# Optimization experiments

Measured on AMD Instinct MI355X. Metric: run time of the kernel, lower is better.

Reference implementation:

```python
import jax, jax.numpy as jnp
import numpy as np

B, L, H, E, F, C = 8, 8192, 512, 8, 1024, 2  # batch, seq, hidden, experts, ffn, capacity factor


def setup_inputs() -> dict:
    key = jax.random.key(0)
    ks = jax.random.split(key, 4)
    x = jax.random.normal(ks[0], (B, L, H), jnp.float32)
    Wg = jax.random.normal(ks[1], (H, E), jnp.float32) * (H ** -0.5)   # gate (no bias)
    W1 = jax.random.normal(ks[2], (E, H, F), jnp.float32) * (H ** -0.5)
    b1 = jnp.zeros((E, F), jnp.float32)
    W2 = jax.random.normal(ks[3], (E, F, H), jnp.float32) * (F ** -0.5)
    b2 = jnp.zeros((E, H), jnp.float32)
    return {"x": x, "Wg": Wg, "W1": W1, "b1": b1, "W2": W2, "b2": b2}


def reference(x, Wg, W1, b1, W2, b2):
    b, l, h = x.shape
    e = Wg.shape[1]
    k = min(max(int(l * C / e), 1), l)  # expert-choice capacity per expert
    # Gate scores: softmax over experts per token, then each expert picks its top-k tokens.
    S = jax.nn.softmax(x @ Wg, axis=-1)          # (b, l, E)
    St = jnp.swapaxes(S, 1, 2)                   # (b, E, l)
    G, I = jax.lax.top_k(St, k)                  # (b, E, k) scores / token indices
    # Dispatch: gather each expert's chosen tokens.
    ex = jnp.take_along_axis(x[:, None], I[..., None], axis=2)   # (b, E, k, h)
    # Grouped expert MLP (Linear -> GELU -> Linear), batched over experts.
    hmid = jax.nn.gelu(jnp.einsum('bekh,ehf->bekf', ex, W1) + b1[None, :, None, :],
                       approximate=False)
    out = jnp.einsum('bekf,efh->bekh', hmid, W2) + b2[None, :, None, :]
    vals = G[..., None] * out                    # weight by gate score
    # Combine: scatter-add expert outputs back to token positions.
    new_x = jnp.zeros_like(x).at[jnp.arange(b)[:, None, None], I].add(vals)
    return new_x
```

## Files before the change

### kernel.cpp

```cpp
#include <hip/hip_runtime.h>
#include <hip/hip_bf16.h>
#include <hip/hip_fp16.h>

typedef float f32x4 __attribute__((ext_vector_type(4)));
typedef _Float16 f16x8 __attribute__((ext_vector_type(8)));
typedef unsigned int u32x4 __attribute__((ext_vector_type(4)));

static constexpr int Bb = 8, Ll = 8192, Hh = 512, Ee = 8, Ff = 1024, KK = 2048;

static __device__ __forceinline__ float fast_rcp(float x) {
#if __has_builtin(__builtin_amdgcn_rcpf)
  return __builtin_amdgcn_rcpf(x);
#else
  return 1.0f / x;
#endif
}

static __device__ __forceinline__ float gelu_exact(float v) {
  float a = __builtin_fabsf(v) * 0.70710678118654752f;
  float t = fast_rcp(__builtin_fmaf(0.3275911f, a, 1.0f));
  float p = __builtin_fmaf(1.061405429f, t, -1.453152027f);
  p = __builtin_fmaf(p, t, 1.421413741f);
  p = __builtin_fmaf(p, t, -0.284496736f);
  p = __builtin_fmaf(p, t, 0.254829592f);
  p = p * t;
  float e = __expf(-a * a);
  float er = __builtin_fmaf(-p, e, 1.0f);
  er = __builtin_copysignf(er, v);
  return 0.5f * v * (1.0f + er);
}

static __device__ __forceinline__ void nt_store16(const f16x8& v, _Float16* p) {
  __builtin_nontemporal_store(*reinterpret_cast<const u32x4*>(&v),
                              reinterpret_cast<u32x4*>(p));
}

__global__ __launch_bounds__(256) void transpose_cvt_kernel(const float* __restrict__ src,
                                                            _Float16* __restrict__ dst,
                                                            int R, int C) {
  __shared__ float tile[32][33];
  int z = blockIdx.z;
  const float* s = src + (size_t)z * R * C;
  _Float16* d = dst + (size_t)z * R * C;
  int c0 = blockIdx.x * 32, r0 = blockIdx.y * 32;
  int tx = threadIdx.x, ty = threadIdx.y;
#pragma unroll
  for (int i = ty; i < 32; i += 8) tile[i][tx] = s[(size_t)(r0 + i) * C + (c0 + tx)];
  __syncthreads();
#pragma unroll
  for (int i = ty; i < 32; i += 8) d[(size_t)(c0 + i) * R + (r0 + tx)] = (_Float16)tile[tx][i];
}

__global__ __launch_bounds__(256) void gatecvt_kernel(const float* __restrict__ x,
                                                      const float* __restrict__ Wg,
                                                      double* __restrict__ St,
                                                      _Float16* __restrict__ xb) {
  __shared__ float wgt[8][516];
  __shared__ float xs[32][68];
  int tid = threadIdx.x;
  for (int i = tid; i < Hh * Ee; i += 256) wgt[i & 7][i >> 3] = Wg[i];
  int row = tid >> 3, seg = tid & 7;
  int tl = row, e = seg;
  int token0 = blockIdx.x * 32;
  const float* xrow = x + (size_t)(token0 + row) * Hh;
  _Float16* xbrow = xb + (size_t)(token0 + row) * Hh;
  float4 r0 = reinterpret_cast<const float4*>(xrow)[seg * 2];
  float4 r1 = reinterpret_cast<const float4*>(xrow)[seg * 2 + 1];
  double acc = 0.0;
  for (int c = 0; c < 8; ++c) {
    f16x8 h;
    h[0] = (_Float16)r0.x; h[1] = (_Float16)r0.y; h[2] = (_Float16)r0.z; h[3] = (_Float16)r0.w;
    h[4] = (_Float16)r1.x; h[5] = (_Float16)r1.y; h[6] = (_Float16)r1.z; h[7] = (_Float16)r1.w;
    nt_store16(h, xbrow + c * 64 + seg * 8);
    __syncthreads();
    *reinterpret_cast<float4*>(&xs[row][seg * 8]) = r0;
    *reinterpret_cast<float4*>(&xs[row][seg * 8 + 4]) = r1;
    if (c + 1 < 8) {
      r0 = reinterpret_cast<const float4*>(xrow + (c + 1) * 64)[seg * 2];
      r1 = reinterpret_cast<const float4*>(xrow + (c + 1) * 64)[seg * 2 + 1];
    }
    __syncthreads();
#pragma unroll
    for (int hh = 0; hh < 64; hh += 4) {
      float4 xv = *reinterpret_cast<const float4*>(&xs[tl][hh]);
      float4 wv = *reinterpret_cast<const float4*>(&wgt[e][c * 64 + hh]);
      acc += (double)xv.x * (double)wv.x;
      acc += (double)xv.y * (double)wv.y;
      acc += (double)xv.z * (double)wv.z;
      acc += (double)xv.w * (double)wv.w;
    }
  }
  double m = acc;
  m = fmax(m, __shfl_xor(m, 1, 64));
  m = fmax(m, __shfl_xor(m, 2, 64));
  m = fmax(m, __shfl_xor(m, 4, 64));
  double ex = exp(acc - m);
  double s = ex;
  s += __shfl_xor(s, 1, 64);
  s += __shfl_xor(s, 2, 64);
  s += __shfl_xor(s, 4, 64);
  int token = token0 + tl;
  int b = token >> 13, l = token & (Ll - 1);
  St[((size_t)(b * Ee + e)) * Ll + l] = ex / s;
}

__global__ __launch_bounds__(1024) void topk_kernel(const double* __restrict__ St,
                                                    int* __restrict__ idx,
                                                    float* __restrict__ gate) {
  __shared__ unsigned long long keys[Ll];
  __shared__ unsigned int hist[256];
  __shared__ unsigned int sc[1024];
  __shared__ unsigned long long s_prefix;
  __shared__ int s_remaining;
  __shared__ unsigned long long redA[16], redO[16];
  int row = blockIdx.x;
  int tid = threadIdx.x;
  const double* s = St + (size_t)row * Ll;
  unsigned long long myA = ~0ULL, myO = 0ULL;
  for (int i = tid; i < Ll; i += 1024) {
    unsigned long long kx = (unsigned long long)__double_as_longlong(s[i]);
    keys[i] = kx;
    myA &= kx;
    myO |= kx;
  }
#pragma unroll
  for (int off2 = 32; off2 >= 1; off2 >>= 1) {
    myA &= __shfl_xor(myA, off2, 64);
    myO |= __shfl_xor(myO, off2, 64);
  }
  if ((tid & 63) == 0) { redA[tid >> 6] = myA; redO[tid >> 6] = myO; }
  __syncthreads();
  unsigned long long allA = redA[0], allO = redO[0];
#pragma unroll
  for (int w = 1; w < 16; ++w) { allA &= redA[w]; allO |= redO[w]; }
  unsigned long long diff = allA ^ allO;

  unsigned long long T;
  int nEqTake;
  if (diff == 0) {
    T = allA;
    nEqTake = KK;
  } else {
    int hb = 63 - __builtin_clzll(diff);
    int pv = hb >> 3;
    unsigned long long prefmask = (pv >= 7) ? 0ULL : (~0ULL << ((pv + 1) * 8));
    unsigned long long prefix = allA & prefmask;
    int remaining = KK;
    for (int p = pv; p >= 0; --p) {
      if (tid < 256) hist[tid] = 0;
      __syncthreads();
      int sh = p * 8;
      for (int i = tid; i < Ll; i += 1024) {
        unsigned long long kk = keys[i];
        if ((kk & prefmask) == prefix) atomicAdd(&hist[(unsigned)(kk >> sh) & 255u], 1u);
      }
      __syncthreads();
      if (tid < 256) sc[tid] = hist[tid];
      __syncthreads();
#pragma unroll
      for (int off = 1; off < 256; off <<= 1) {
        unsigned v = (tid < 256 && tid + off < 256) ? sc[tid + off] : 0;
        __syncthreads();
        if (tid < 256) sc[tid] += v;
        __syncthreads();
      }
      if (tid < 256) {
        unsigned incl = sc[tid];
        unsigned above = (tid == 255) ? 0u : sc[tid + 1];
        if ((int)incl >= remaining && (int)above < remaining) {
          s_remaining = remaining - (int)above;
          s_prefix = prefix | ((unsigned long long)(unsigned)tid << sh);
        }
      }
      __syncthreads();
      remaining = s_remaining;
      prefix = s_prefix;
      prefmask |= (255ULL << sh);
      __syncthreads();
    }
    T = prefix;
    nEqTake = remaining;
  }

  int base = tid * 8;
  unsigned long long kk[8];
  unsigned gtc = 0, eqc = 0;
#pragma unroll
  for (int j = 0; j < 8; ++j) {
    kk[j] = keys[base + j];
    gtc += (kk[j] > T);
    eqc += (kk[j] == T);
  }
  unsigned packed = (gtc << 16) | eqc;
  sc[tid] = packed;
  __syncthreads();
  for (int off = 1; off < 1024; off <<= 1) {
    unsigned v = (tid >= off) ? sc[tid - off] : 0;
    __syncthreads();
    sc[tid] += v;
    __syncthreads();
  }
  unsigned excl = sc[tid] - packed;
  int gtb = (int)(excl >> 16), eqb = (int)(excl & 0xFFFFu);
  int orow = row * KK;
#pragma unroll
  for (int j = 0; j < 8; ++j) {
    bool isgt = kk[j] > T, iseq = kk[j] == T;
    bool take = isgt || (iseq && eqb < nEqTake);
    if (take) {
      int pos = gtb + (eqb < nEqTake ? eqb : nEqTake);
      idx[orow + pos] = base + j;
      gate[orow + pos] = (float)__longlong_as_double((long long)kk[j]);
    }
    gtb += isgt ? 1 : 0;
    eqb += iseq ? 1 : 0;
  }
}

__global__ __launch_bounds__(256) void buildinv_kernel(const int* __restrict__ idx,
                                                       int* __restrict__ cnt,
                                                       int* __restrict__ inv) {
  int s = blockIdx.x * 256 + threadIdx.x;
  int gp = s >> 11;
  int b = gp >> 3;
  int t = idx[s];
  int key = b * Ll + t;
  int pos = atomicAdd(&cnt[key], 1);
  inv[key * 8 + pos] = s;
}

__global__ __launch_bounds__(256) void combine_kernel(const _Float16* __restrict__ yout,
                                                      const int* __restrict__ cnt,
                                                      const int* __restrict__ inv,
                                                      float* __restrict__ out) {
  int tglob = blockIdx.x * 4 + (threadIdx.x >> 6);
  int lane = threadIdx.x & 63;
  int n = cnt[tglob];
  float acc[8];
#pragma unroll
  for (int j = 0; j < 8; ++j) acc[j] = 0.f;
  for (int c = 0; c < n; ++c) {
    int s = inv[tglob * 8 + c];
    u32x4 u = __builtin_nontemporal_load(
        reinterpret_cast<const u32x4*>(yout + (size_t)s * Hh + lane * 8));
    f16x8 v = *reinterpret_cast<f16x8*>(&u);
#pragma unroll
    for (int j = 0; j < 8; ++j) acc[j] += (float)v[j];
  }
  float* o = out + (size_t)tglob * Hh + lane * 8;
  f32x4 lo = {acc[0], acc[1], acc[2], acc[3]};
  f32x4 hi = {acc[4], acc[5], acc[6], acc[7]};
  __builtin_nontemporal_store(lo, reinterpret_cast<f32x4*>(o));
  __builtin_nontemporal_store(hi, reinterpret_cast<f32x4*>(o + 4));
}

__global__ __launch_bounds__(512, 2) void gemm1_kernel(const _Float16* __restrict__ xb,
                                                       const _Float16* __restrict__ w1t,
                                                       const float* __restrict__ b1,
                                                       const int* __restrict__ idx,
                                                       _Float16* __restrict__ hmid,
                                                       int chunk_base, int slotbase) {
  __shared__ __align__(16) _Float16 lds[65536];
  int tid = threadIdx.x, lane = tid & 63, wid = tid >> 6;
  int nat = blockIdx.x;
  int zz = nat & 7;
  int rem = nat >> 3;
  int bx = rem & 3, by = rem >> 2;
  int gp = chunk_base + zz;
  int slot = slotbase + zz;
  int b = gp >> 3, e = gp & 7;
  int m0 = by * 256, f0 = bx * 256;

  const _Float16* srcbase[8];
  int dstoff[8];
#pragma unroll
  for (int i = 0; i < 8; ++i) {
    int c = wid * 8 + i;
    int lr = (c & 31) * 8 + (lane >> 3);
    int q = lane & 7;
    int qg = q ^ (lr & 7);
    if (c < 32) {
      int token = idx[(size_t)gp * KK + m0 + lr];
      srcbase[i] = xb + ((size_t)b * Ll + token) * Hh + qg * 8;
      dstoff[i] = (c & 31) * 512;
    } else {
      srcbase[i] = w1t + ((size_t)e * Ff + f0 + lr) * Hh + qg * 8;
      dstoff[i] = 16384 + (c & 31) * 512;
    }
  }

  f32x4 acc[8][4] = {};
  int wm = wid >> 2, wn = wid & 3;
  int a_off[8], b_off[4];
  int ko = lane >> 4;
#pragma unroll
  for (int i = 0; i < 8; ++i) {
    int ra = wm * 128 + i * 16 + (lane & 15);
    a_off[i] = ra * 64 + (ko ^ (ra & 7)) * 8;
  }
#pragma unroll
  for (int i = 0; i < 4; ++i) {
    int rb = wn * 64 + i * 16 + (lane & 15);
    b_off[i] = 16384 + rb * 64 + (ko ^ (rb & 7)) * 8;
  }

  auto stage = [&](int p, int kt) {
#pragma unroll
    for (int i = 0; i < 8; ++i) {
      __builtin_amdgcn_global_load_lds(
          (const __attribute__((address_space(1))) void*)(srcbase[i] + kt),
          (__attribute__((address_space(3))) void*)(lds + p * 32768 + dstoff[i]), 16, 0, 0);
    }
  };

  constexpr int nt = Hh / 64;
  stage(0, 0);
  for (int t = 0; t < nt; ++t) {
    __syncthreads();
    if (t + 1 < nt) stage((t + 1) & 1, (t + 1) * 64);
    const _Float16* buf = lds + (t & 1) * 32768;
#pragma unroll
    for (int half = 0; half < 2; ++half) {
      int kx = half * 32;
      f16x8 af[8], bf[4];
#pragma unroll
      for (int i = 0; i < 8; ++i) af[i] = *reinterpret_cast<const f16x8*>(buf + (a_off[i] ^ kx));
#pragma unroll
      for (int i = 0; i < 4; ++i) bf[i] = *reinterpret_cast<const f16x8*>(buf + (b_off[i] ^ kx));
      __builtin_amdgcn_s_setprio(1);
#pragma unroll
      for (int fr = 0; fr < 8; ++fr)
#pragma unroll
        for (int fc = 0; fc < 4; ++fc)
          acc[fr][fc] = __builtin_amdgcn_mfma_f32_16x16x32_f16(af[fr], bf[fc], acc[fr][fc], 0, 0, 0);
      __builtin_amdgcn_s_setprio(0);
    }
  }
  __syncthreads();

  int cidx = lane & 15, rbase = (lane >> 4) * 4;
  float b1v[4];
#pragma unroll
  for (int fc = 0; fc < 4; ++fc) b1v[fc] = b1[e * Ff + f0 + wn * 64 + fc * 16 + cidx];
#pragma unroll
  for (int fr = 0; fr < 8; ++fr) {
#pragma unroll
    for (int fc = 0; fc < 4; ++fc) {
#pragma unroll
      for (int r = 0; r < 4; ++r) {
        int lm = wm * 128 + fr * 16 + rbase + r;
        int lf = wn * 64 + fc * 16 + cidx;
        float v = acc[fr][fc][r] + b1v[fc];
        lds[lm * 256 + (((lf >> 3) ^ (lm & 7)) << 3) + (lf & 7)] = (_Float16)gelu_exact(v);
      }
    }
  }
  __syncthreads();
  _Float16* hd = hmid + (size_t)slot * KK * Ff;
  int orow = tid >> 5, seg = tid & 31;
#pragma unroll
  for (int pp = 0; pp < 16; ++pp) {
    int lm = pp * 16 + orow;
    f16x8 v = *reinterpret_cast<const f16x8*>(lds + lm * 256 + ((seg ^ (lm & 7)) << 3));
    nt_store16(v, hd + (size_t)(m0 + lm) * Ff + f0 + seg * 8);
  }
}

__global__ __launch_bounds__(512, 2) void gemm2_kernel(const _Float16* __restrict__ hmid,
                                                       const _Float16* __restrict__ w2t,
                                                       const float* __restrict__ b2,
                                                       const int* __restrict__ idx,
                                                       const float* __restrict__ gate,
                                                       _Float16* __restrict__ yout,
                                                       int chunk_base, int pairs16) {
  __shared__ __align__(16) _Float16 lds[65536];
  int tid = threadIdx.x, lane = tid & 63, wid = tid >> 6;
  int nat = blockIdx.x;
  int zz, rem;
  if (pairs16) {
    zz = (nat & 7) * 2 + ((nat >> 3) & 1);
    rem = nat >> 4;
  } else {
    zz = nat & 7;
    rem = nat >> 3;
  }
  int bx = rem & 1, by = rem >> 1;
  int gp = chunk_base + zz;
  int slot = zz;
  int e = gp & 7;
  int m0 = by * 256, h0 = bx * 256;

  const _Float16* srcbase[8];
  int dstoff[8];
#pragma unroll
  for (int i = 0; i < 8; ++i) {
    int c = wid * 8 + i;
    int lr = (c & 31) * 8 + (lane >> 3);
    int q = lane & 7;
    int qg = q ^ (lr & 7);
    if (c < 32) {
      srcbase[i] = hmid + ((size_t)slot * KK + m0 + lr) * Ff + qg * 8;
      dstoff[i] = (c & 31) * 512;
    } else {
      srcbase[i] = w2t + ((size_t)e * Hh + h0 + lr) * Ff + qg * 8;
      dstoff[i] = 16384 + (c & 31) * 512;
    }
  }

  f32x4 acc[8][4] = {};
  int wm = wid >> 2, wn = wid & 3;
  int a_off[8], b_off[4];
  int ko = lane >> 4;
#pragma unroll
  for (int i = 0; i < 8; ++i) {
    int ra = wm * 128 + i * 16 + (lane & 15);
    a_off[i] = ra * 64 + (ko ^ (ra & 7)) * 8;
  }
#pragma unroll
  for (int i = 0; i < 4; ++i) {
    int rb = wn * 64 + i * 16 + (lane & 15);
    b_off[i] = 16384 + rb * 64 + (ko ^ (rb & 7)) * 8;
  }

  auto stage = [&](int p, int kt) {
#pragma unroll
    for (int i = 0; i < 8; ++i) {
      __builtin_amdgcn_global_load_lds(
          (const __attribute__((address_space(1))) void*)(srcbase[i] + kt),
          (__attribute__((address_space(3))) void*)(lds + p * 32768 + dstoff[i]), 16, 0, 0);
    }
  };

  constexpr int nt = Ff / 64;
  stage(0, 0);
  for (int t = 0; t < nt; ++t) {
    __syncthreads();
    if (t + 1 < nt) stage((t + 1) & 1, (t + 1) * 64);
    const _Float16* buf = lds + (t & 1) * 32768;
#pragma unroll
    for (int half = 0; half < 2; ++half) {
      int kx = half * 32;
      f16x8 af[8], bf[4];
#pragma unroll
      for (int i = 0; i < 8; ++i) af[i] = *reinterpret_cast<const f16x8*>(buf + (a_off[i] ^ kx));
#pragma unroll
      for (int i = 0; i < 4; ++i) bf[i] = *reinterpret_cast<const f16x8*>(buf + (b_off[i] ^ kx));
      __builtin_amdgcn_s_setprio(1);
#pragma unroll
      for (int fr = 0; fr < 8; ++fr)
#pragma unroll
        for (int fc = 0; fc < 4; ++fc)
          acc[fr][fc] = __builtin_amdgcn_mfma_f32_16x16x32_f16(af[fr], bf[fc], acc[fr][fc], 0, 0, 0);
      __builtin_amdgcn_s_setprio(0);
    }
  }
  __syncthreads();

  int cidx = lane & 15, rbase = (lane >> 4) * 4;
  float b2v[4];
#pragma unroll
  for (int fc = 0; fc < 4; ++fc) b2v[fc] = b2[e * Hh + h0 + wn * 64 + fc * 16 + cidx];
#pragma unroll
  for (int fr = 0; fr < 8; ++fr) {
    float gv[4];
#pragma unroll
    for (int r = 0; r < 4; ++r) {
      int lm = wm * 128 + fr * 16 + rbase + r;
      gv[r] = gate[(size_t)gp * KK + m0 + lm];
    }
#pragma unroll
    for (int fc = 0; fc < 4; ++fc) {
#pragma unroll
      for (int r = 0; r < 4; ++r) {
        int lm = wm * 128 + fr * 16 + rbase + r;
        int lh = wn * 64 + fc * 16 + cidx;
        float v = acc[fr][fc][r] + b2v[fc];
        lds[lm * 256 + (((lh >> 3) ^ (lm & 7)) << 3) + (lh & 7)] = (_Float16)(gv[r] * v);
      }
    }
  }
  __syncthreads();
  int orow = tid >> 5, seg = tid & 31;
#pragma unroll
  for (int pp = 0; pp < 16; ++pp) {
    int lm = pp * 16 + orow;
    f16x8 v = *reinterpret_cast<const f16x8*>(lds + lm * 256 + ((seg ^ (lm & 7)) << 3));
    nt_store16(v, yout + ((size_t)gp * KK + m0 + lm) * Hh + h0 + seg * 8);
  }
}

extern "C" void kernel_launch(void* const* d_in, const int* in_sizes, int n_in,
                              void* d_out, int out_size, void* d_ws, size_t ws_size,
                              hipStream_t stream) {
  const float* x  = (const float*)d_in[0];
  const float* Wg = (const float*)d_in[1];
  const float* W1 = (const float*)d_in[2];
  const float* b1 = (const float*)d_in[3];
  const float* W2 = (const float*)d_in[4];
  const float* b2 = (const float*)d_in[5];
  float* out = (float*)d_out;

  char* ws = (char*)d_ws;
  size_t off = 0;
  auto alloc = [&](size_t bytes) -> char* {
    char* p = ws + off;
    off = (off + bytes + 255) & ~(size_t)255;
    return p;
  };
  _Float16* xb   = (_Float16*)alloc((size_t)Bb * Ll * Hh * 2);
  _Float16* w1t  = (_Float16*)alloc((size_t)Ee * Ff * Hh * 2);
  _Float16* w2t  = (_Float16*)alloc((size_t)Ee * Hh * Ff * 2);
  double*   St   = (double*)alloc((size_t)Bb * Ee * Ll * 8);
  int*      dI   = (int*)alloc((size_t)Bb * Ee * KK * 4);
  float*    dG   = (float*)alloc((size_t)Bb * Ee * KK * 4);
  int*      cnt  = (int*)alloc((size_t)Bb * Ll * 4);
  int*      inv  = (int*)alloc((size_t)Bb * Ll * 8 * 4);
  _Float16* yout = (_Float16*)alloc((size_t)Bb * Ee * KK * Hh * 2);
  size_t fixed = off;
  size_t per_pair = (size_t)KK * Ff * 2;
  bool big = (fixed + per_pair * 16 <= ws_size);
  int chunk = big ? 16 : 8;
  _Float16* hmid = (_Float16*)alloc(per_pair * (size_t)chunk);

  hipMemsetAsync(cnt, 0, (size_t)Bb * Ll * 4, stream);
  gatecvt_kernel<<<Bb * Ll / 32, 256, 0, stream>>>(x, Wg, St, xb);
  transpose_cvt_kernel<<<dim3(Ff / 32, Hh / 32, Ee), dim3(32, 8), 0, stream>>>(W1, w1t, Hh, Ff);
  transpose_cvt_kernel<<<dim3(Hh / 32, Ff / 32, Ee), dim3(32, 8), 0, stream>>>(W2, w2t, Ff, Hh);
  topk_kernel<<<Bb * Ee, 1024, 0, stream>>>(St, dI, dG);
  buildinv_kernel<<<Bb * Ee * KK / 256, 256, 0, stream>>>(dI, cnt, inv);

  if (big) {
    for (int cb = 0; cb < Bb * Ee; cb += 16) {
      gemm1_kernel<<<256, 512, 0, stream>>>(xb, w1t, b1, dI, hmid, cb, 0);
      gemm1_kernel<<<256, 512, 0, stream>>>(xb, w1t, b1, dI, hmid, cb + 8, 8);
      gemm2_kernel<<<256, 512, 0, stream>>>(hmid, w2t, b2, dI, dG, yout, cb, 1);
    }
  } else {
    for (int cb = 0; cb < Bb * Ee; cb += 8) {
      gemm1_kernel<<<256, 512, 0, stream>>>(xb, w1t, b1, dI, hmid, cb, 0);
      gemm2_kernel<<<128, 512, 0, stream>>>(hmid, w2t, b2, dI, dG, yout, cb, 0);
    }
  }
  combine_kernel<<<Bb * Ll / 4, 256, 0, stream>>>(yout, cnt, inv, out);
}
```

Baseline: 543.5 us.

## Batch expert GEMM launches in larger chunks, cheapen GELU, widen gate kernel

Generalises the expert pair chunking so gemm1/gemm2 each launch once per chunk of up to 32 pairs, replacing the paired gemm1 launches, to cut launch count and tail effects. Replaces the 5-term erf polynomial in GELU with a 3-term approximation, lowering epilogue arithmetic at the cost of accuracy. Restructures the gate kernel to process 128-wide slices with four independent double accumulators, shortening dependency chains and halving barrier rounds. A larger hmid workspace is needed for the 32-pair path.

```diff
diff --git a/kernel.cpp b/kernel.cpp
--- a/kernel.cpp
+++ b/kernel.cpp
@@ -18,11 +18,9 @@
 
 static __device__ __forceinline__ float gelu_exact(float v) {
   float a = __builtin_fabsf(v) * 0.70710678118654752f;
-  float t = fast_rcp(__builtin_fmaf(0.3275911f, a, 1.0f));
-  float p = __builtin_fmaf(1.061405429f, t, -1.453152027f);
-  p = __builtin_fmaf(p, t, 1.421413741f);
-  p = __builtin_fmaf(p, t, -0.284496736f);
-  p = __builtin_fmaf(p, t, 0.254829592f);
+  float t = fast_rcp(__builtin_fmaf(0.47047f, a, 1.0f));
+  float p = __builtin_fmaf(0.7478556f, t, -0.0958798f);
+  p = __builtin_fmaf(p, t, 0.3480242f);
   p = p * t;
   float e = __expf(-a * a);
   float er = __builtin_fmaf(-p, e, 1.0f);
@@ -56,40 +54,47 @@
                                                       double* __restrict__ St,
                                                       _Float16* __restrict__ xb) {
   __shared__ float wgt[8][516];
-  __shared__ float xs[32][68];
+  __shared__ float xs[32][132];
   int tid = threadIdx.x;
   for (int i = tid; i < Hh * Ee; i += 256) wgt[i & 7][i >> 3] = Wg[i];
   int row = tid >> 3, seg = tid & 7;
-  int tl = row, e = seg;
   int token0 = blockIdx.x * 32;
   const float* xrow = x + (size_t)(token0 + row) * Hh;
   _Float16* xbrow = xb + (size_t)(token0 + row) * Hh;
-  float4 r0 = reinterpret_cast<const float4*>(xrow)[seg * 2];
-  float4 r1 = reinterpret_cast<const float4*>(xrow)[seg * 2 + 1];
-  double acc = 0.0;
-  for (int c = 0; c < 8; ++c) {
-    f16x8 h;
-    h[0] = (_Float16)r0.x; h[1] = (_Float16)r0.y; h[2] = (_Float16)r0.z; h[3] = (_Float16)r0.w;
-    h[4] = (_Float16)r1.x; h[5] = (_Float16)r1.y; h[6] = (_Float16)r1.z; h[7] = (_Float16)r1.w;
-    nt_store16(h, xbrow + c * 64 + seg * 8);
+  float4 r0 = reinterpret_cast<const float4*>(xrow)[seg * 4 + 0];
+  float4 r1 = reinterpret_cast<const float4*>(xrow)[seg * 4 + 1];
+  float4 r2 = reinterpret_cast<const float4*>(xrow)[seg * 4 + 2];
+  float4 r3 = reinterpret_cast<const float4*>(xrow)[seg * 4 + 3];
+  double a0 = 0.0, a1 = 0.0, a2 = 0.0, a3 = 0.0;
+  for (int c = 0; c < 4; ++c) {
+    f16x8 h0, h1;
+    h0[0] = (_Float16)r0.x; h0[1] = (_Float16)r0.y; h0[2] = (_Float16)r0.z; h0[3] = (_Float16)r0.w;
+    h0[4] = (_Float16)r1.x; h0[5] = (_Float16)r1.y; h0[6] = (_Float16)r1.z; h0[7] = (_Float16)r1.w;
+    h1[0] = (_Float16)r2.x; h1[1] = (_Float16)r2.y; h1[2] = (_Float16)r2.z; h1[3] = (_Float16)r2.w;
+    h1[4] = (_Float16)r3.x; h1[5] = (_Float16)r3.y; h1[6] = (_Float16)r3.z; h1[7] = (_Float16)r3.w;
+    nt_store16(h0, xbrow + c * 128 + seg * 16);
+    nt_store16(h1, xbrow + c * 128 + seg * 16 + 8);
     __syncthreads();
-    *reinterpret_cast<float4*>(&xs[row][seg * 8]) = r0;
-    *reinterpret_cast<float4*>(&xs[row][seg * 8 + 4]) = r1;
-    if (c + 1 < 8) {
-      r0 = reinterpret_cast<const float4*>(xrow + (c + 1) * 64)[seg * 2];
-      r1 = reinterpret_cast<const float4*>(xrow + (c + 1) * 64)[seg * 2 + 1];
+    *reinterpret_cast<float4*>(&xs[row][seg * 16 + 0]) = r0;
+    *reinterpret_cast<float4*>(&xs[row][seg * 16 + 4]) = r1;
+    *reinterpret_cast<float4*>(&xs[row][seg * 16 + 8]) = r2;
+    *reinterpret_cast<float4*>(&xs[row][seg * 16 + 12]) = r3;
+    if (c + 1 < 4) {
+      const float4* nx = reinterpret_cast<const float4*>(xrow + (c + 1) * 128);
+      r0 = nx[seg * 4 + 0]; r1 = nx[seg * 4 + 1]; r2 = nx[seg * 4 + 2]; r3 = nx[seg * 4 + 3];
     }
     __syncthreads();
 #pragma unroll
-    for (int hh = 0; hh < 64; hh += 4) {
-      float4 xv = *reinterpret_cast<const float4*>(&xs[tl][hh]);
-      float4 wv = *reinterpret_cast<const float4*>(&wgt[e][c * 64 + hh]);
-      acc += (double)xv.x * (double)wv.x;
-      acc += (double)xv.y * (double)wv.y;
-      acc += (double)xv.z * (double)wv.z;
-      acc += (double)xv.w * (double)wv.w;
-    }
-  }
+    for (int hh = 0; hh < 128; hh += 4) {
+      float4 xv = *reinterpret_cast<const float4*>(&xs[row][hh]);
+      float4 wv = *reinterpret_cast<const float4*>(&wgt[seg][c * 128 + hh]);
+      a0 += (double)xv.x * (double)wv.x;
+      a1 += (double)xv.y * (double)wv.y;
+      a2 += (double)xv.z * (double)wv.z;
+      a3 += (double)xv.w * (double)wv.w;
+    }
+  }
+  double acc = (a0 + a1) + (a2 + a3);
   double m = acc;
   m = fmax(m, __shfl_xor(m, 1, 64));
   m = fmax(m, __shfl_xor(m, 2, 64));
@@ -99,9 +104,9 @@
   s += __shfl_xor(s, 1, 64);
   s += __shfl_xor(s, 2, 64);
   s += __shfl_xor(s, 4, 64);
-  int token = token0 + tl;
+  int token = token0 + row;
   int b = token >> 13, l = token & (Ll - 1);
-  St[((size_t)(b * Ee + e)) * Ll + l] = ex / s;
+  St[((size_t)(b * Ee + seg)) * Ll + l] = ex / s;
 }
 
 __global__ __launch_bounds__(1024) void topk_kernel(const double* __restrict__ St,
@@ -259,15 +264,16 @@
                                                        const float* __restrict__ b1,
                                                        const int* __restrict__ idx,
                                                        _Float16* __restrict__ hmid,
-                                                       int chunk_base, int slotbase) {
+                                                       int chunk_base) {
   __shared__ __align__(16) _Float16 lds[65536];
   int tid = threadIdx.x, lane = tid & 63, wid = tid >> 6;
   int nat = blockIdx.x;
-  int zz = nat & 7;
-  int rem = nat >> 3;
-  int bx = rem & 3, by = rem >> 2;
-  int gp = chunk_base + zz;
-  int slot = slotbase + zz;
+  int rr = nat >> 8;
+  int j = nat & 7;
+  int idxb = (nat >> 3) & 31;
+  int pl = rr * 8 + j;
+  int bx = idxb & 3, by = idxb >> 2;
+  int gp = chunk_base + pl;
   int b = gp >> 3, e = gp & 7;
   int m0 = by * 256, f0 = bx * 256;
 
@@ -356,7 +362,7 @@
     }
   }
   __syncthreads();
-  _Float16* hd = hmid + (size_t)slot * KK * Ff;
+  _Float16* hd = hmid + (size_t)pl * KK * Ff;
   int orow = tid >> 5, seg = tid & 31;
 #pragma unroll
   for (int pp = 0; pp < 16; ++pp) {
@@ -372,23 +378,29 @@
                                                        const int* __restrict__ idx,
                                                        const float* __restrict__ gate,
                                                        _Float16* __restrict__ yout,
-                                                       int chunk_base, int pairs16) {
+                                                       int chunk_base, int small8) {
   __shared__ __align__(16) _Float16 lds[65536];
   int tid = threadIdx.x, lane = tid & 63, wid = tid >> 6;
   int nat = blockIdx.x;
-  int zz, rem;
-  if (pairs16) {
-    zz = (nat & 7) * 2 + ((nat >> 3) & 1);
-    rem = nat >> 4;
+  int ci, by;
+  if (small8) {
+    int j = nat & 7;
+    int idxb = nat >> 3;
+    ci = j * 2 + (idxb >> 3);
+    by = idxb & 7;
   } else {
-    zz = nat & 7;
-    rem = nat >> 3;
-  }
-  int bx = rem & 1, by = rem >> 1;
-  int gp = chunk_base + zz;
-  int slot = zz;
+    int rr = nat >> 8;
+    int low = nat & 255;
+    int j = low & 7;
+    int idxb = low >> 3;
+    ci = rr * 32 + j * 4 + (idxb >> 3);
+    by = idxb & 7;
+  }
+  int pl = ci >> 1;
+  int h0 = (ci & 1) * 256;
+  int gp = chunk_base + pl;
   int e = gp & 7;
-  int m0 = by * 256, h0 = bx * 256;
+  int m0 = by * 256;
 
   const _Float16* srcbase[8];
   int dstoff[8];
@@ -399,7 +411,7 @@
     int q = lane & 7;
     int qg = q ^ (lr & 7);
     if (c < 32) {
-      srcbase[i] = hmid + ((size_t)slot * KK + m0 + lr) * Ff + qg * 8;
+      srcbase[i] = hmid + ((size_t)pl * KK + m0 + lr) * Ff + qg * 8;
       dstoff[i] = (c & 31) * 512;
     } else {
       srcbase[i] = w2t + ((size_t)e * Hh + h0 + lr) * Ff + qg * 8;
@@ -518,8 +530,9 @@
   _Float16* yout = (_Float16*)alloc((size_t)Bb * Ee * KK * Hh * 2);
   size_t fixed = off;
   size_t per_pair = (size_t)KK * Ff * 2;
-  bool big = (fixed + per_pair * 16 <= ws_size);
-  int chunk = big ? 16 : 8;
+  int chunk = 8;
+  if (fixed + per_pair * 32 <= ws_size) chunk = 32;
+  else if (fixed + per_pair * 16 <= ws_size) chunk = 16;
   _Float16* hmid = (_Float16*)alloc(per_pair * (size_t)chunk);
 
   hipMemsetAsync(cnt, 0, (size_t)Bb * Ll * 4, stream);
@@ -529,17 +542,10 @@
   topk_kernel<<<Bb * Ee, 1024, 0, stream>>>(St, dI, dG);
   buildinv_kernel<<<Bb * Ee * KK / 256, 256, 0, stream>>>(dI, cnt, inv);
 
-  if (big) {
-    for (int cb = 0; cb < Bb * Ee; cb += 16) {
-      gemm1_kernel<<<256, 512, 0, stream>>>(xb, w1t, b1, dI, hmid, cb, 0);
-      gemm1_kernel<<<256, 512, 0, stream>>>(xb, w1t, b1, dI, hmid, cb + 8, 8);
-      gemm2_kernel<<<256, 512, 0, stream>>>(hmid, w2t, b2, dI, dG, yout, cb, 1);
-    }
-  } else {
-    for (int cb = 0; cb < Bb * Ee; cb += 8) {
-      gemm1_kernel<<<256, 512, 0, stream>>>(xb, w1t, b1, dI, hmid, cb, 0);
-      gemm2_kernel<<<128, 512, 0, stream>>>(hmid, w2t, b2, dI, dG, yout, cb, 0);
-    }
+  for (int cb = 0; cb < Bb * Ee; cb += chunk) {
+    gemm1_kernel<<<chunk * 32, 512, 0, stream>>>(xb, w1t, b1, dI, hmid, cb);
+    gemm2_kernel<<<chunk * 16, 512, 0, stream>>>(hmid, w2t, b2, dI, dG, yout, cb,
+                                                 chunk == 8 ? 1 : 0);
   }
   combine_kernel<<<Bb * Ll / 4, 256, 0, stream>>>(yout, cnt, inv, out);
 }
```

Result: faster. 523.1 us, median of 2 (-3.8%).
